# Kernel tuning notes

Measured on AMD Instinct MI355X. Metric: run time of the kernel, lower is better.

## Reference

```python
import jax, jax.numpy as jnp
import numpy as np

EPS = 1e-9          # numerator epsilon from the original code
COS_EPS = 1e-8      # torch cosine_similarity clamps norms at 1e-8


def setup_inputs() -> dict:
    key = jax.random.key(0)
    kx, ky = jax.random.split(key)
    N, D = 8192, 1024
    x = jax.random.normal(kx, (N, D), dtype=jnp.float32)
    y = jax.random.randint(ky, (N,), 0, 10, dtype=jnp.int64)
    T = jnp.ones((1,), dtype=jnp.float32)
    return {"x": x, "y": y, "T": T}


def reference(x, y, T):
    # Soft Nearest Neighbor Loss with cosine distance, vectorized.
    # fits(i, j) = exp(-(1 - cos_sim(x_i, x_j)) / T)
    N = x.shape[0]
    norms = jnp.maximum(jnp.linalg.norm(x, axis=1, keepdims=True), COS_EPS)
    xn = x / norms                                   # [N, D] unit vectors
    sim = xn @ xn.T                                  # [N, N] cosine similarity
    f = jnp.exp(-(1.0 - sim) / T[0])                 # [N, N] fits

    off_diag = ~jnp.eye(N, dtype=bool)               # exclude i == j
    same = (y[:, None] == y[None, :]) & off_diag     # same-label pairs

    top = jnp.sum(jnp.where(same, f, 0.0), axis=1)   # [N]
    bot = jnp.sum(jnp.where(off_diag, f, 0.0), axis=1)
    loss = -jnp.mean(jnp.log((top + EPS) / bot))
    return loss
```

## Files before the change

kernel.cpp:

```cpp
#include <hip/hip_runtime.h>

#define NROWS 8192
#define DDIM  1024

typedef short  bf16x8 __attribute__((ext_vector_type(8)));
typedef float  f32x4  __attribute__((ext_vector_type(4)));
typedef unsigned short ushort_t;

__device__ __forceinline__ ushort_t f2bf(float f) {
    union { float f; unsigned u; } v; v.f = f;
    unsigned r = v.u + 0x7fffu + ((v.u >> 16) & 1u);
    return (ushort_t)(r >> 16);
}

#define GLD(gp, lp)                                                        \
    __builtin_amdgcn_global_load_lds(                                      \
        (const __attribute__((address_space(1))) void*)(gp),               \
        (__attribute__((address_space(3))) void*)(lp), 16, 0, 0)

__global__ __launch_bounds__(256) void snnl_normalize(
    const float* __restrict__ x, ushort_t* __restrict__ xn,
    float* __restrict__ top, float* __restrict__ bot, float* __restrict__ out)
{
    const int row = (int)blockIdx.x;
    const int tid = (int)threadIdx.x;
    if (tid == 0) {
        top[row] = 0.0f;
        bot[row] = 0.0f;
        if (row == 0) out[0] = 0.0f;
    }
    const float4 v = ((const float4*)(x + (size_t)row * DDIM))[tid];
    float ss = v.x * v.x + v.y * v.y + v.z * v.z + v.w * v.w;
#pragma unroll
    for (int m = 32; m >= 1; m >>= 1) ss += __shfl_xor(ss, m);
    __shared__ float ws4[4];
    if ((tid & 63) == 0) ws4[tid >> 6] = ss;
    __syncthreads();
    const float tot = ws4[0] + ws4[1] + ws4[2] + ws4[3];
    const float inv = 1.0f / fmaxf(sqrtf(tot), 1e-8f);
    ushort4 o;
    o.x = f2bf(v.x * inv);
    o.y = f2bf(v.y * inv);
    o.z = f2bf(v.z * inv);
    o.w = f2bf(v.w * inv);
    ((ushort4*)(xn + (size_t)row * DDIM))[tid] = o;
}

__global__ __launch_bounds__(256, 4) void snnl_main(
    const ushort_t* __restrict__ xn, const int* __restrict__ y,
    const float* __restrict__ T,
    float* __restrict__ top, float* __restrict__ bot)
{
    const int bid = (int)blockIdx.x;
    int rem = (bid & 7) * 260 + (bid >> 3);
    int p = 0, q = 0;
    {
        bool done = false;
        for (int qq = 0; qq < 8 && !done; ++qq) {
            for (int pp = 0; pp <= qq; ++pp) {
                const int c = (pp == qq) ? 36 : 64;
                if (rem < c) { p = pp; q = qq; done = true; break; }
                rem -= c;
            }
        }
    }
    int ti, tj;
    if (p == q) {
        int t = rem; tj = 7;
        for (int cc = 0; cc < 8; ++cc) {
            if (t <= cc) { tj = cc; break; }
            t -= (cc + 1);
        }
        ti = t;
    } else {
        ti = rem & 7; tj = rem >> 3;
    }
    const int bi = p * 8 + ti;
    const int bj = q * 8 + tj;
    const bool strict = (bi < bj);

    __shared__ char smem[32768];
    __shared__ int  yrow_s[128];
    __shared__ int  ycol_s[128];

    const int tid  = (int)threadIdx.x;
    const int lane = tid & 63;
    const int w    = tid >> 6;
    const int wr   = w >> 1;
    const int wc   = w & 1;
    const int i0   = bi * 128;
    const int j0   = bj * 128;

    if (tid < 128) yrow_s[tid] = y[i0 + tid];
    else           ycol_s[tid - 128] = y[j0 + tid - 128];

    const float invT = 1.0f / T[0];

    const int  rr  = tid >> 3;
    const int  scb = (((tid & 7) ^ (rr & 7)) << 4);
    const char* const xb = (const char*)xn;

    const int c0 = (((lane >> 4) << 4)) ^ ((lane & 7) << 4);
    int arow[4], brow[4];
#pragma unroll
    for (int mi = 0; mi < 4; ++mi) arow[mi] = (wr * 64 + mi * 16 + (lane & 15)) * 128;
#pragma unroll
    for (int ni = 0; ni < 4; ++ni) brow[ni] = 16384 + (wc * 64 + ni * 16 + (lane & 15)) * 128;

    const f32x4 zero4 = {0.0f, 0.0f, 0.0f, 0.0f};
    f32x4 acc[4][4];
#pragma unroll
    for (int mi = 0; mi < 4; ++mi)
#pragma unroll
        for (int ni = 0; ni < 4; ++ni) acc[mi][ni] = zero4;

    for (int kt = 0; kt < 16; ++kt) {
        const size_t kb = ((size_t)kt << 7) + (size_t)scb;
#pragma unroll
        for (int qq = 0; qq < 4; ++qq)
            GLD(xb + (((size_t)(i0 + qq * 32 + rr)) << 11) + kb,
                smem + (qq << 12) + (tid << 4));
#pragma unroll
        for (int qq = 0; qq < 4; ++qq)
            GLD(xb + (((size_t)(j0 + qq * 32 + rr)) << 11) + kb,
                smem + 16384 + (qq << 12) + (tid << 4));
        __syncthreads();

#pragma unroll
        for (int ks = 0; ks < 2; ++ks) {
            const int cks = c0 ^ (ks << 6);
            bf16x8 af[4], bfr[4];
#pragma unroll
            for (int mi = 0; mi < 4; ++mi)
                af[mi] = *(const bf16x8*)(smem + arow[mi] + cks);
#pragma unroll
            for (int ni = 0; ni < 4; ++ni)
                bfr[ni] = *(const bf16x8*)(smem + brow[ni] + cks);
#pragma unroll
            for (int mi = 0; mi < 4; ++mi)
#pragma unroll
                for (int ni = 0; ni < 4; ++ni)
                    acc[mi][ni] = __builtin_amdgcn_mfma_f32_16x16x32_bf16(
                        af[mi], bfr[ni], acc[mi][ni], 0, 0, 0);
        }
        __syncthreads();
    }

    int yjv[4], jgv[4];
#pragma unroll
    for (int ni = 0; ni < 4; ++ni) {
        const int jloc = wc * 64 + ni * 16 + (lane & 15);
        yjv[ni] = ycol_s[jloc];
        jgv[ni] = j0 + jloc;
    }
    float ct[4], cb[4];
#pragma unroll
    for (int ni = 0; ni < 4; ++ni) { ct[ni] = 0.0f; cb[ni] = 0.0f; }

#pragma unroll
    for (int mi = 0; mi < 4; ++mi) {
#pragma unroll
        for (int r = 0; r < 4; ++r) {
            const int il = wr * 64 + mi * 16 + ((lane >> 4) << 2) + r;
            const int ig = i0 + il;
            const int yi = yrow_s[il];
            float ba = 0.0f, ta = 0.0f;
#pragma unroll
            for (int ni = 0; ni < 4; ++ni) {
                const float fv = __expf((acc[mi][ni][r] - 1.0f) * invT);
                const bool  sm = (yi == yjv[ni]);
                const float bv = (ig != jgv[ni]) ? fv : 0.0f;
                const float tv = sm ? bv : 0.0f;
                ba += bv;  ta += tv;
                cb[ni] += bv;  ct[ni] += tv;
            }
            ta += __shfl_xor(ta, 1); ta += __shfl_xor(ta, 2);
            ta += __shfl_xor(ta, 4); ta += __shfl_xor(ta, 8);
            ba += __shfl_xor(ba, 1); ba += __shfl_xor(ba, 2);
            ba += __shfl_xor(ba, 4); ba += __shfl_xor(ba, 8);
            if ((lane & 15) == 0) {
                atomicAdd(&top[ig], ta);
                atomicAdd(&bot[ig], ba);
            }
        }
    }

    if (strict) {
#pragma unroll
        for (int ni = 0; ni < 4; ++ni) {
            float tv = ct[ni], bv = cb[ni];
            tv += __shfl_xor(tv, 16); tv += __shfl_xor(tv, 32);
            bv += __shfl_xor(bv, 16); bv += __shfl_xor(bv, 32);
            if (lane < 16) {
                atomicAdd(&top[jgv[ni]], tv);
                atomicAdd(&bot[jgv[ni]], bv);
            }
        }
    }
}

__global__ __launch_bounds__(256) void snnl_loss(
    const float* __restrict__ top, const float* __restrict__ bot,
    float* __restrict__ out)
{
    const int tid = (int)threadIdx.x;
    const int i   = (int)blockIdx.x * 256 + tid;
    float s = __logf((top[i] + 1e-9f) / bot[i]);
#pragma unroll
    for (int m = 32; m >= 1; m >>= 1) s += __shfl_xor(s, m);
    __shared__ float w4[4];
    if ((tid & 63) == 0) w4[tid >> 6] = s;
    __syncthreads();
    if (tid == 0)
        atomicAdd(out, -(w4[0] + w4[1] + w4[2] + w4[3]) * (1.0f / (float)NROWS));
}

extern "C" void kernel_launch(void* const* d_in, const int* in_sizes, int n_in,
                              void* d_out, int out_size, void* d_ws, size_t ws_size,
                              hipStream_t stream)
{
    const float* x = (const float*)d_in[0];
    const int*   y = (const int*)d_in[1];
    const float* T = (const float*)d_in[2];
    float* out = (float*)d_out;

    char* ws = (char*)d_ws;
    ushort_t* xn  = (ushort_t*)ws;
    float*    top = (float*)(ws + (size_t)16 * 1024 * 1024);
    float*    bot = top + NROWS;

    snnl_normalize<<<NROWS, 256, 0, stream>>>(x, xn, top, bot, out);
    snnl_main<<<2080, 256, 0, stream>>>(xn, y, T, top, bot);
    snnl_loss<<<NROWS / 256, 256, 0, stream>>>(top, bot, out);
}
```

Baseline: 180.2 us.

## Use 256x128 tiles in main kernel and one wave per row in normalize

```diff
diff --git a/kernel.cpp b/kernel.cpp
--- a/kernel.cpp
+++ b/kernel.cpp
@@ -22,65 +22,68 @@
     const float* __restrict__ x, ushort_t* __restrict__ xn,
     float* __restrict__ top, float* __restrict__ bot, float* __restrict__ out)
 {
-    const int row = (int)blockIdx.x;
-    const int tid = (int)threadIdx.x;
-    if (tid == 0) {
-        top[row] = 0.0f;
-        bot[row] = 0.0f;
-        if (row == 0) out[0] = 0.0f;
-    }
-    const float4 v = ((const float4*)(x + (size_t)row * DDIM))[tid];
-    float ss = v.x * v.x + v.y * v.y + v.z * v.z + v.w * v.w;
+    const int tid  = (int)threadIdx.x;
+    const int lane = tid & 63;
+    const int row  = (int)blockIdx.x * 4 + (tid >> 6);
+    if (lane == 0) { top[row] = 0.0f; bot[row] = 0.0f; }
+    if (row == 0 && lane == 0) out[0] = 0.0f;
+
+    const float4* xr = (const float4*)(x + (size_t)row * DDIM);
+    float4 v[4];
+#pragma unroll
+    for (int st = 0; st < 4; ++st) v[st] = xr[st * 64 + lane];
+    float ss = 0.0f;
+#pragma unroll
+    for (int st = 0; st < 4; ++st)
+        ss += v[st].x * v[st].x + v[st].y * v[st].y
+            + v[st].z * v[st].z + v[st].w * v[st].w;
 #pragma unroll
     for (int m = 32; m >= 1; m >>= 1) ss += __shfl_xor(ss, m);
-    __shared__ float ws4[4];
-    if ((tid & 63) == 0) ws4[tid >> 6] = ss;
-    __syncthreads();
-    const float tot = ws4[0] + ws4[1] + ws4[2] + ws4[3];
-    const float inv = 1.0f / fmaxf(sqrtf(tot), 1e-8f);
-    ushort4 o;
-    o.x = f2bf(v.x * inv);
-    o.y = f2bf(v.y * inv);
-    o.z = f2bf(v.z * inv);
-    o.w = f2bf(v.w * inv);
-    ((ushort4*)(xn + (size_t)row * DDIM))[tid] = o;
-}
-
-__global__ __launch_bounds__(256, 4) void snnl_main(
+    const float inv = 1.0f / fmaxf(sqrtf(ss), 1e-8f);
+    ushort4* xo = (ushort4*)(xn + (size_t)row * DDIM);
+#pragma unroll
+    for (int st = 0; st < 4; ++st) {
+        ushort4 o;
+        o.x = f2bf(v[st].x * inv);
+        o.y = f2bf(v[st].y * inv);
+        o.z = f2bf(v[st].z * inv);
+        o.w = f2bf(v[st].w * inv);
+        xo[st * 64 + lane] = o;
+    }
+}
+
+__global__ __launch_bounds__(512, 4) void snnl_main(
     const ushort_t* __restrict__ xn, const int* __restrict__ y,
     const float* __restrict__ T,
     float* __restrict__ top, float* __restrict__ bot)
 {
     const int bid = (int)blockIdx.x;
-    int rem = (bid & 7) * 260 + (bid >> 3);
-    int p = 0, q = 0;
+    int rem = (bid & 7) * 132 + (bid >> 3);
+    int P = 0, Q = 0;
     {
         bool done = false;
         for (int qq = 0; qq < 8 && !done; ++qq) {
             for (int pp = 0; pp <= qq; ++pp) {
-                const int c = (pp == qq) ? 36 : 64;
-                if (rem < c) { p = pp; q = qq; done = true; break; }
+                const int c = (pp == qq) ? 20 : 32;
+                if (rem < c) { P = pp; Q = qq; done = true; break; }
                 rem -= c;
             }
         }
     }
-    int ti, tj;
-    if (p == q) {
-        int t = rem; tj = 7;
-        for (int cc = 0; cc < 8; ++cc) {
-            if (t <= cc) { tj = cc; break; }
-            t -= (cc + 1);
-        }
-        ti = t;
+    int l, m;
+    if (P == Q) {
+        if      (rem < 8)  { l = 0; m = rem; }
+        else if (rem < 14) { l = 1; m = rem - 8 + 2; }
+        else if (rem < 18) { l = 2; m = rem - 14 + 4; }
+        else               { l = 3; m = rem - 18 + 6; }
     } else {
-        ti = rem & 7; tj = rem >> 3;
-    }
-    const int bi = p * 8 + ti;
-    const int bj = q * 8 + tj;
-    const bool strict = (bi < bj);
-
-    __shared__ char smem[32768];
-    __shared__ int  yrow_s[128];
+        l = rem & 3; m = rem >> 2;
+    }
+    const int bi2 = P * 4 + l;
+    const int bj  = Q * 8 + m;
+
+    __shared__ char smem[49152];
+    __shared__ int  yrow_s[256];
     __shared__ int  ycol_s[128];
 
     const int tid  = (int)threadIdx.x;
@@ -88,11 +91,16 @@
     const int w    = tid >> 6;
     const int wr   = w >> 1;
     const int wc   = w & 1;
-    const int i0   = bi * 128;
+    const int i0   = bi2 * 256;
     const int j0   = bj * 128;
 
-    if (tid < 128) yrow_s[tid] = y[i0 + tid];
-    else           ycol_s[tid - 128] = y[j0 + tid - 128];
+    const int  s      = wr >> 1;
+    const int  bi_s   = 2 * bi2 + s;
+    const bool valid  = (bi_s <= bj);
+    const bool strict = (bi_s <  bj);
+
+    if (tid < 256)       yrow_s[tid] = y[i0 + tid];
+    else if (tid < 384)  ycol_s[tid - 256] = y[j0 + tid - 256];
 
     const float invT = 1.0f / T[0];
 
@@ -105,7 +113,7 @@
 #pragma unroll
     for (int mi = 0; mi < 4; ++mi) arow[mi] = (wr * 64 + mi * 16 + (lane & 15)) * 128;
 #pragma unroll
-    for (int ni = 0; ni < 4; ++ni) brow[ni] = 16384 + (wc * 64 + ni * 16 + (lane & 15)) * 128;
+    for (int ni = 0; ni < 4; ++ni) brow[ni] = 32768 + (wc * 64 + ni * 16 + (lane & 15)) * 128;
 
     const f32x4 zero4 = {0.0f, 0.0f, 0.0f, 0.0f};
     f32x4 acc[4][4];
@@ -118,12 +126,12 @@
         const size_t kb = ((size_t)kt << 7) + (size_t)scb;
 #pragma unroll
         for (int qq = 0; qq < 4; ++qq)
-            GLD(xb + (((size_t)(i0 + qq * 32 + rr)) << 11) + kb,
-                smem + (qq << 12) + (tid << 4));
-#pragma unroll
-        for (int qq = 0; qq < 4; ++qq)
-            GLD(xb + (((size_t)(j0 + qq * 32 + rr)) << 11) + kb,
-                smem + 16384 + (qq << 12) + (tid << 4));
+            GLD(xb + (((size_t)(i0 + qq * 64 + rr)) << 11) + kb,
+                smem + (qq << 13) + (tid << 4));
+#pragma unroll
+        for (int qq = 0; qq < 2; ++qq)
+            GLD(xb + (((size_t)(j0 + qq * 64 + rr)) << 11) + kb,
+                smem + 32768 + (qq << 13) + (tid << 4));
         __syncthreads();
 
 #pragma unroll
@@ -157,30 +165,32 @@
 #pragma unroll
     for (int ni = 0; ni < 4; ++ni) { ct[ni] = 0.0f; cb[ni] = 0.0f; }
 
-#pragma unroll
-    for (int mi = 0; mi < 4; ++mi) {
-#pragma unroll
-        for (int r = 0; r < 4; ++r) {
-            const int il = wr * 64 + mi * 16 + ((lane >> 4) << 2) + r;
-            const int ig = i0 + il;
-            const int yi = yrow_s[il];
-            float ba = 0.0f, ta = 0.0f;
-#pragma unroll
-            for (int ni = 0; ni < 4; ++ni) {
-                const float fv = __expf((acc[mi][ni][r] - 1.0f) * invT);
-                const bool  sm = (yi == yjv[ni]);
-                const float bv = (ig != jgv[ni]) ? fv : 0.0f;
-                const float tv = sm ? bv : 0.0f;
-                ba += bv;  ta += tv;
-                cb[ni] += bv;  ct[ni] += tv;
-            }
-            ta += __shfl_xor(ta, 1); ta += __shfl_xor(ta, 2);
-            ta += __shfl_xor(ta, 4); ta += __shfl_xor(ta, 8);
-            ba += __shfl_xor(ba, 1); ba += __shfl_xor(ba, 2);
-            ba += __shfl_xor(ba, 4); ba += __shfl_xor(ba, 8);
-            if ((lane & 15) == 0) {
-                atomicAdd(&top[ig], ta);
-                atomicAdd(&bot[ig], ba);
+    if (valid) {
+#pragma unroll
+        for (int mi = 0; mi < 4; ++mi) {
+#pragma unroll
+            for (int r = 0; r < 4; ++r) {
+                const int il = wr * 64 + mi * 16 + ((lane >> 4) << 2) + r;
+                const int ig = i0 + il;
+                const int yi = yrow_s[il];
+                float ba = 0.0f, ta = 0.0f;
+#pragma unroll
+                for (int ni = 0; ni < 4; ++ni) {
+                    const float fv = __expf((acc[mi][ni][r] - 1.0f) * invT);
+                    const bool  sm = (yi == yjv[ni]);
+                    const float bv = (ig != jgv[ni]) ? fv : 0.0f;
+                    const float tv = sm ? bv : 0.0f;
+                    ba += bv;  ta += tv;
+                    cb[ni] += bv;  ct[ni] += tv;
+                }
+                ta += __shfl_xor(ta, 1); ta += __shfl_xor(ta, 2);
+                ta += __shfl_xor(ta, 4); ta += __shfl_xor(ta, 8);
+                ba += __shfl_xor(ba, 1); ba += __shfl_xor(ba, 2);
+                ba += __shfl_xor(ba, 4); ba += __shfl_xor(ba, 8);
+                if ((lane & 15) == 0) {
+                    atomicAdd(&top[ig], ta);
+                    atomicAdd(&bot[ig], ba);
+                }
             }
         }
     }
@@ -229,7 +239,7 @@
     float*    top = (float*)(ws + (size_t)16 * 1024 * 1024);
     float*    bot = top + NROWS;
 
-    snnl_normalize<<<NROWS, 256, 0, stream>>>(x, xn, top, bot, out);
-    snnl_main<<<2080, 256, 0, stream>>>(xn, y, T, top, bot);
+    snnl_normalize<<<NROWS / 4, 256, 0, stream>>>(x, xn, top, bot, out);
+    snnl_main<<<1056, 512, 0, stream>>>(xn, y, T, top, bot);
     snnl_loss<<<NROWS / 256, 256, 0, stream>>>(top, bot, out);
 }
```

After: 193.0 us. 1.07x slower.

## Normalize one row per wavefront and lower main kernel occupancy target

Applied to the files above, without the earlier changes.

```diff
diff --git a/kernel.cpp b/kernel.cpp
--- a/kernel.cpp
+++ b/kernel.cpp
@@ -22,31 +22,37 @@
     const float* __restrict__ x, ushort_t* __restrict__ xn,
     float* __restrict__ top, float* __restrict__ bot, float* __restrict__ out)
 {
-    const int row = (int)blockIdx.x;
-    const int tid = (int)threadIdx.x;
-    if (tid == 0) {
-        top[row] = 0.0f;
-        bot[row] = 0.0f;
-        if (row == 0) out[0] = 0.0f;
-    }
-    const float4 v = ((const float4*)(x + (size_t)row * DDIM))[tid];
-    float ss = v.x * v.x + v.y * v.y + v.z * v.z + v.w * v.w;
+    const int tid  = (int)threadIdx.x;
+    const int lane = tid & 63;
+    const int row  = (int)blockIdx.x * 4 + (tid >> 6);
+    if (lane == 0) { top[row] = 0.0f; bot[row] = 0.0f; }
+    if (row == 0 && lane == 0) out[0] = 0.0f;
+
+    const float4* xr = (const float4*)(x + (size_t)row * DDIM);
+    float4 v[4];
+#pragma unroll
+    for (int st = 0; st < 4; ++st) v[st] = xr[st * 64 + lane];
+    float ss = 0.0f;
+#pragma unroll
+    for (int st = 0; st < 4; ++st)
+        ss += v[st].x * v[st].x + v[st].y * v[st].y
+            + v[st].z * v[st].z + v[st].w * v[st].w;
 #pragma unroll
     for (int m = 32; m >= 1; m >>= 1) ss += __shfl_xor(ss, m);
-    __shared__ float ws4[4];
-    if ((tid & 63) == 0) ws4[tid >> 6] = ss;
-    __syncthreads();
-    const float tot = ws4[0] + ws4[1] + ws4[2] + ws4[3];
-    const float inv = 1.0f / fmaxf(sqrtf(tot), 1e-8f);
-    ushort4 o;
-    o.x = f2bf(v.x * inv);
-    o.y = f2bf(v.y * inv);
-    o.z = f2bf(v.z * inv);
-    o.w = f2bf(v.w * inv);
-    ((ushort4*)(xn + (size_t)row * DDIM))[tid] = o;
-}
-
-__global__ __launch_bounds__(256, 4) void snnl_main(
+    const float inv = 1.0f / fmaxf(sqrtf(ss), 1e-8f);
+    ushort4* xo = (ushort4*)(xn + (size_t)row * DDIM);
+#pragma unroll
+    for (int st = 0; st < 4; ++st) {
+        ushort4 o;
+        o.x = f2bf(v[st].x * inv);
+        o.y = f2bf(v[st].y * inv);
+        o.z = f2bf(v[st].z * inv);
+        o.w = f2bf(v[st].w * inv);
+        xo[st * 64 + lane] = o;
+    }
+}
+
+__global__ __launch_bounds__(256, 2) void snnl_main(
     const ushort_t* __restrict__ xn, const int* __restrict__ y,
     const float* __restrict__ T,
     float* __restrict__ top, float* __restrict__ bot)
@@ -79,7 +85,7 @@
     const int bj = q * 8 + tj;
     const bool strict = (bi < bj);
 
-    __shared__ char smem[32768];
+    __shared__ char smem[57344];
     __shared__ int  yrow_s[128];
     __shared__ int  ycol_s[128];
 
@@ -229,7 +235,7 @@
     float*    top = (float*)(ws + (size_t)16 * 1024 * 1024);
     float*    bot = top + NROWS;
 
-    snnl_normalize<<<NROWS, 256, 0, stream>>>(x, xn, top, bot, out);
+    snnl_normalize<<<NROWS / 4, 256, 0, stream>>>(x, xn, top, bot, out);
     snnl_main<<<2080, 256, 0, stream>>>(xn, y, T, top, bot);
     snnl_loss<<<NROWS / 256, 256, 0, stream>>>(top, bot, out);
 }
```

Measured after the change: 189.6 us. 5.2% more time.
